# Performance work log

Hardware: AMD Instinct MI355X
Metric: run time of the kernel (lower is better)

## Reference

```python
import jax, jax.numpy as jnp
import numpy as np

NUM_HEADS = 8
EMBED_DIM = 512
HEAD_DIM = EMBED_DIM // NUM_HEADS
SCALE = 1.0 / (HEAD_DIM ** 0.5)


def setup_inputs() -> dict:
    key = jax.random.key(0)
    ks = jax.random.split(key, 8)
    std = 0.02
    x = jax.random.normal(ks[0], (2, 1024, EMBED_DIM), dtype=jnp.float32)
    wq = jax.random.normal(ks[1], (HEAD_DIM, HEAD_DIM), dtype=jnp.float32) * std
    wk = jax.random.normal(ks[2], (HEAD_DIM, HEAD_DIM), dtype=jnp.float32) * std
    wv = jax.random.normal(ks[3], (HEAD_DIM, HEAD_DIM), dtype=jnp.float32) * std
    w1 = jax.random.normal(ks[4], (2 * EMBED_DIM, EMBED_DIM), dtype=jnp.float32) * std
    b1 = jnp.zeros((2 * EMBED_DIM,), dtype=jnp.float32)
    w2 = jax.random.normal(ks[5], (EMBED_DIM, 2 * EMBED_DIM), dtype=jnp.float32) * std
    b2 = jnp.zeros((EMBED_DIM,), dtype=jnp.float32)
    return {"x": x, "wq": wq, "wk": wk, "wv": wv,
            "w1": w1, "b1": b1, "w2": w2, "b2": b2}


def reference(x, wq, wk, wv, w1, b1, w2, b2):
    b, n, e = x.shape
    # rearrange 'b n (h d) -> b (n h) d': heads are folded into the sequence dim,
    # so attention mixes across n*h tokens of head_dim features.
    xh = x.reshape(b, n * NUM_HEADS, HEAD_DIM)  # [b, n*h, d]
    q = jnp.einsum('bsd,ed->bse', xh, wq)
    k = jnp.einsum('bsd,ed->bse', xh, wk)
    v = jnp.einsum('bsd,ed->bse', xh, wv)
    scores = jnp.einsum('bse,bte->bst', q, k) * SCALE  # [b, n*h, n*h]
    attn = jax.nn.softmax(scores, axis=-1)
    out = jnp.einsum('bst,btd->bsd', attn, v)  # [b, n*h, d]
    out = out.reshape(b, n, e)  # 'b (n h) d -> b n (h d)'
    # Mlp: Linear -> GELU(exact) -> Linear (dropout rates are 0)
    h = jax.nn.gelu(jnp.einsum('bne,fe->bnf', out, w1) + b1, approximate=False)
    out = jnp.einsum('bnf,ef->bne', h, w2) + b2
    return attn, out
```

## Files before the change

kernel.cpp:

```cpp
#include <hip/hip_runtime.h>
#include <hip/hip_bf16.h>

typedef __bf16 bf16;
typedef bf16 bf16x8 __attribute__((ext_vector_type(8)));
typedef float f32x16 __attribute__((ext_vector_type(16)));

#define MFMA(a,b,c) __builtin_amdgcn_mfma_f32_32x32x16_bf16(a,b,c,0,0,0)

constexpr int S = 8192;
constexpr long long SB = (long long)S * S;
constexpr long long ATTN_ELEMS = 2 * SB;

__global__ __launch_bounds__(64) void qkv_kernel(
    const float* __restrict__ x, const float* __restrict__ wq,
    const float* __restrict__ wk, const float* __restrict__ wv,
    bf16* __restrict__ qb, bf16* __restrict__ kb, bf16* __restrict__ vt)
{
  __shared__ bf16 vtl[64 * 34];
  const int lane = threadIdx.x;
  const int lo = lane & 31, hi = lane >> 5;
  const int m0 = blockIdx.x * 32;

  bf16x8 af[4];
  {
    const float* xr = x + (size_t)(m0 + lo) * 64 + hi * 8;
#pragma unroll
    for (int s = 0; s < 4; ++s) {
      const float* p = xr + 16 * s;
#pragma unroll
      for (int j = 0; j < 8; ++j) af[s][j] = (bf16)p[j];
    }
  }

  const float* wmats[3] = {wq, wk, wv};
#pragma unroll 1
  for (int mat = 0; mat < 3; ++mat) {
    const float* w = wmats[mat];
#pragma unroll 1
    for (int h = 0; h < 2; ++h) {
      f32x16 acc = {};
#pragma unroll
      for (int s = 0; s < 4; ++s) {
        const float* p = w + (size_t)(32 * h + lo) * 64 + hi * 8 + 16 * s;
        bf16x8 bfr;
#pragma unroll
        for (int j = 0; j < 8; ++j) bfr[j] = (bf16)p[j];
        acc = MFMA(af[s], bfr, acc);
      }
      const int col = 32 * h + lo;
#pragma unroll
      for (int i = 0; i < 16; ++i) {
        int row = (i & 3) + 8 * (i >> 2) + 4 * hi;
        float v = acc[i];
        if (mat == 0) {
          qb[(size_t)(m0 + row) * 64 + col] = (bf16)(v * 0.125f);
        } else if (mat == 1) {
          kb[(size_t)(m0 + row) * 64 + col] = (bf16)v;
        } else {
          vtl[col * 34 + row] = (bf16)v;
        }
      }
    }
  }
  __syncthreads();
  const int b = m0 >> 13;
  const int t0 = m0 & 8191;
#pragma unroll 1
  for (int i = 0; i < 32; ++i) {
    int d = 2 * i + hi;
    vt[(size_t)b * (64 * 8192) + (size_t)d * 8192 + t0 + lo] = vtl[d * 34 + lo];
  }
}

__global__ __launch_bounds__(256) void attn_kernel(
    const bf16* __restrict__ qb, const bf16* __restrict__ kb,
    const bf16* __restrict__ vt, float* __restrict__ attn_out,
    float* __restrict__ o_ws)
{
  __shared__ bf16 plds[4 * 32 * 40];
  __shared__ float olds[32 * 65];
  __shared__ float l4[4 * 32];
  __shared__ float linv[32];

  const int tid = threadIdx.x;
  const int lane = tid & 63;
  const int wt = tid >> 6;
  const int lo = lane & 31, hi = lane >> 5;

  const int bx = blockIdx.x;
  const int g = bx >> 3, r = bx & 7;
  const int b = r >> 2;
  const int m0 = (g * 4 + (r & 3)) * 32;

  for (int i = tid; i < 32 * 65; i += 256) olds[i] = 0.0f;

  bf16x8 qf[4];
  {
    const bf16* qr = qb + ((size_t)b * S + m0 + lo) * 64 + hi * 8;
#pragma unroll
    for (int s = 0; s < 4; ++s) qf[s] = *(const bf16x8*)(qr + 16 * s);
  }
  const bf16* kbase = kb + (size_t)b * S * 64;
  const bf16* vbase = vt + (size_t)b * 64 * S;

  float lsum[16];
#pragma unroll
  for (int i = 0; i < 16; ++i) lsum[i] = 0.0f;
#pragma unroll 1
  for (int c = 0; c < 64; ++c) {
    const int t0 = c * 128 + wt * 32;
    f32x16 acc = {};
#pragma unroll
    for (int s = 0; s < 4; ++s) {
      bf16x8 kf = *(const bf16x8*)(kbase + (size_t)(t0 + lo) * 64 + hi * 8 + 16 * s);
      acc = MFMA(qf[s], kf, acc);
    }
#pragma unroll
    for (int i = 0; i < 16; ++i) lsum[i] += __expf(acc[i]);
  }
#pragma unroll
  for (int i = 0; i < 16; ++i) {
    float v = lsum[i];
#pragma unroll
    for (int m = 1; m <= 16; m <<= 1) v += __shfl_xor(v, m);
    lsum[i] = v;
  }
#pragma unroll
  for (int i = 0; i < 16; ++i)
    if (lo == i) l4[wt * 32 + (i & 3) + 8 * (i >> 2) + 4 * hi] = lsum[i];
  __syncthreads();
  if (tid < 32)
    linv[tid] = 1.0f / (l4[tid] + l4[32 + tid] + l4[64 + tid] + l4[96 + tid]);
  __syncthreads();

  float linv_r[16];
#pragma unroll
  for (int i = 0; i < 16; ++i)
    linv_r[i] = linv[(i & 3) + 8 * (i >> 2) + 4 * hi];

  f32x16 oacc0 = {}, oacc1 = {};
  bf16* pw = plds + wt * 1280;
  float* aout = attn_out + (size_t)b * SB + (size_t)m0 * S;
#pragma unroll 1
  for (int c = 0; c < 64; ++c) {
    const int t0 = c * 128 + wt * 32;
    f32x16 acc = {};
#pragma unroll
    for (int s = 0; s < 4; ++s) {
      bf16x8 kf = *(const bf16x8*)(kbase + (size_t)(t0 + lo) * 64 + hi * 8 + 16 * s);
      acc = MFMA(qf[s], kf, acc);
    }
#pragma unroll
    for (int i = 0; i < 16; ++i) {
      int row = (i & 3) + 8 * (i >> 2) + 4 * hi;
      float p = __expf(acc[i]) * linv_r[i];
      __builtin_nontemporal_store(p, aout + (size_t)row * S + t0 + lo);
      pw[row * 40 + lo] = (bf16)p;
    }
#pragma unroll
    for (int s = 0; s < 2; ++s) {
      bf16x8 pf = *(const bf16x8*)(pw + lo * 40 + 16 * s + 8 * hi);
      bf16x8 v0 = *(const bf16x8*)(vbase + (size_t)lo * S + t0 + 16 * s + 8 * hi);
      bf16x8 v1 = *(const bf16x8*)(vbase + (size_t)(32 + lo) * S + t0 + 16 * s + 8 * hi);
      oacc0 = MFMA(pf, v0, oacc0);
      oacc1 = MFMA(pf, v1, oacc1);
    }
  }
#pragma unroll
  for (int i = 0; i < 16; ++i) {
    int row = (i & 3) + 8 * (i >> 2) + 4 * hi;
    atomicAdd(&olds[row * 65 + lo], oacc0[i]);
    atomicAdd(&olds[row * 65 + 32 + lo], oacc1[i]);
  }
  __syncthreads();
#pragma unroll
  for (int k = 0; k < 8; ++k) {
    int idx = k * 256 + tid;
    int row = idx >> 6, col = idx & 63;
    o_ws[((size_t)b * S + m0 + row) * 64 + col] = olds[row * 65 + col];
  }
}

__device__ inline float gelu_exact(float v) {
  return 0.5f * v * (1.0f + erff(v * 0.70710678118654752f));
}

__global__ __launch_bounds__(256) void mlp1_kernel(
    const float* __restrict__ o_ws, const float* __restrict__ w1,
    const float* __restrict__ b1, bf16* __restrict__ hhi, bf16* __restrict__ hlo)
{
  const int tid = threadIdx.x;
  const int lane = tid & 63;
  const int wid = tid >> 6;
  const int lo = lane & 31, hi = lane >> 5;
  const int mt = blockIdx.x & 31, nt = blockIdx.x >> 5;
  const int m0 = mt * 64 + (wid & 1) * 32;
  const int f0 = nt * 64 + (wid >> 1) * 32;

  f32x16 acc = {};
  const float* arow = o_ws + (size_t)(m0 + lo) * 512 + hi * 8;
  const float* brow = w1 + (size_t)(f0 + lo) * 512 + hi * 8;
#pragma unroll 1
  for (int s = 0; s < 32; ++s) {
    const float* pa = arow + 16 * s;
    const float* pb = brow + 16 * s;
    bf16x8 ah, al, bh, bl;
#pragma unroll
    for (int j = 0; j < 8; ++j) {
      float a = pa[j];  bf16 h = (bf16)a;  ah[j] = h;  al[j] = (bf16)(a - (float)h);
      float bv = pb[j]; bf16 g = (bf16)bv; bh[j] = g;  bl[j] = (bf16)(bv - (float)g);
    }
    acc = MFMA(ah, bh, acc);
    acc = MFMA(ah, bl, acc);
    acc = MFMA(al, bh, acc);
  }
  const int f = f0 + lo;
  const float bias = b1[f];
#pragma unroll
  for (int i = 0; i < 16; ++i) {
    int m = m0 + (i & 3) + 8 * (i >> 2) + 4 * hi;
    float gv = gelu_exact(acc[i] + bias);
    bf16 h = (bf16)gv;
    hhi[(size_t)m * 1024 + f] = h;
    hlo[(size_t)m * 1024 + f] = (bf16)(gv - (float)h);
  }
}

__global__ __launch_bounds__(256) void mlp2_kernel(
    const bf16* __restrict__ hhi, const bf16* __restrict__ hlo,
    const float* __restrict__ w2, const float* __restrict__ b2,
    float* __restrict__ out2)
{
  const int tid = threadIdx.x;
  const int lane = tid & 63;
  const int wid = tid >> 6;
  const int lo = lane & 31, hi = lane >> 5;
  const int mt = blockIdx.x & 31, nt = blockIdx.x >> 5;
  const int m0 = mt * 64 + (wid & 1) * 32;
  const int e0 = nt * 64 + (wid >> 1) * 32;

  f32x16 acc = {};
  const bf16* ahr = hhi + (size_t)(m0 + lo) * 1024 + hi * 8;
  const bf16* alr = hlo + (size_t)(m0 + lo) * 1024 + hi * 8;
  const float* brow = w2 + (size_t)(e0 + lo) * 1024 + hi * 8;
#pragma unroll 1
  for (int s = 0; s < 64; ++s) {
    bf16x8 ah = *(const bf16x8*)(ahr + 16 * s);
    bf16x8 al = *(const bf16x8*)(alr + 16 * s);
    const float* pb = brow + 16 * s;
    bf16x8 bh, bl;
#pragma unroll
    for (int j = 0; j < 8; ++j) {
      float bv = pb[j]; bf16 g = (bf16)bv; bh[j] = g; bl[j] = (bf16)(bv - (float)g);
    }
    acc = MFMA(ah, bh, acc);
    acc = MFMA(al, bh, acc);
    acc = MFMA(ah, bl, acc);
  }
  const int e = e0 + lo;
  const float bias = b2[e];
#pragma unroll
  for (int i = 0; i < 16; ++i) {
    int m = m0 + (i & 3) + 8 * (i >> 2) + 4 * hi;
    out2[(size_t)m * 512 + e] = acc[i] + bias;
  }
}

extern "C" void kernel_launch(void* const* d_in, const int* in_sizes, int n_in,
                              void* d_out, int out_size, void* d_ws, size_t ws_size,
                              hipStream_t stream) {
  const float* x  = (const float*)d_in[0];
  const float* wq = (const float*)d_in[1];
  const float* wk = (const float*)d_in[2];
  const float* wv = (const float*)d_in[3];
  const float* w1 = (const float*)d_in[4];
  const float* b1 = (const float*)d_in[5];
  const float* w2 = (const float*)d_in[6];
  const float* b2 = (const float*)d_in[7];
  float* out = (float*)d_out;

  char* ws = (char*)d_ws;
  bf16* qb   = (bf16*)(ws);
  bf16* kb   = (bf16*)(ws + (2u << 20));
  bf16* vtb  = (bf16*)(ws + (4u << 20));
  float* ob  = (float*)(ws + (6u << 20));
  bf16* hhi  = (bf16*)(ws + (10u << 20));
  bf16* hlo  = (bf16*)(ws + (14u << 20));

  qkv_kernel<<<512, 64, 0, stream>>>(x, wq, wk, wv, qb, kb, vtb);
  attn_kernel<<<512, 256, 0, stream>>>(qb, kb, vtb, out, ob);
  mlp1_kernel<<<512, 256, 0, stream>>>(ob, w1, b1, hhi, hlo);
  mlp2_kernel<<<256, 256, 0, stream>>>(hhi, hlo, w2, b2, out + ATTN_ELEMS);
}
```

Measured before the change: 753.3 us.

## Transpose QK^T MFMA so each lane owns a query row and stores vectorized

Swaps the MFMA operand order so the score tile is computed transposed, making each lane hold 16 key columns of a single query row. This lets the row-sum reduction collapse to a single cross-half shuffle, uses one scalar inverse-sum per lane, and turns the attention-probability writes into 16-byte nontemporal vector stores and 8-byte LDS stores. K and V loads for the tile are also issued up front to hide latency. The main target is the huge fp32 attention-matrix store traffic, which was previously scalar and strided.

```diff
diff --git a/kernel.cpp b/kernel.cpp
--- a/kernel.cpp
+++ b/kernel.cpp
@@ -3,7 +3,9 @@
 
 typedef __bf16 bf16;
 typedef bf16 bf16x8 __attribute__((ext_vector_type(8)));
+typedef bf16 bf16x4 __attribute__((ext_vector_type(4)));
 typedef float f32x16 __attribute__((ext_vector_type(16)));
+typedef float f32x4 __attribute__((ext_vector_type(4)));
 
 #define MFMA(a,b,c) __builtin_amdgcn_mfma_f32_32x32x16_bf16(a,b,c,0,0,0)
 
@@ -103,67 +105,82 @@
   const bf16* kbase = kb + (size_t)b * S * 64;
   const bf16* vbase = vt + (size_t)b * 64 * S;
 
-  float lsum[16];
-#pragma unroll
-  for (int i = 0; i < 16; ++i) lsum[i] = 0.0f;
+  float e0 = 0.0f, e1 = 0.0f, e2 = 0.0f, e3 = 0.0f;
 #pragma unroll 1
   for (int c = 0; c < 64; ++c) {
     const int t0 = c * 128 + wt * 32;
+    const bf16* krow = kbase + (size_t)(t0 + lo) * 64 + hi * 8;
     f32x16 acc = {};
 #pragma unroll
     for (int s = 0; s < 4; ++s) {
-      bf16x8 kf = *(const bf16x8*)(kbase + (size_t)(t0 + lo) * 64 + hi * 8 + 16 * s);
-      acc = MFMA(qf[s], kf, acc);
-    }
-#pragma unroll
-    for (int i = 0; i < 16; ++i) lsum[i] += __expf(acc[i]);
-  }
-#pragma unroll
-  for (int i = 0; i < 16; ++i) {
-    float v = lsum[i];
-#pragma unroll
-    for (int m = 1; m <= 16; m <<= 1) v += __shfl_xor(v, m);
-    lsum[i] = v;
-  }
-#pragma unroll
-  for (int i = 0; i < 16; ++i)
-    if (lo == i) l4[wt * 32 + (i & 3) + 8 * (i >> 2) + 4 * hi] = lsum[i];
+      bf16x8 kf = *(const bf16x8*)(krow + 16 * s);
+      acc = MFMA(kf, qf[s], acc);
+    }
+#pragma unroll
+    for (int i = 0; i < 16; i += 4) {
+      e0 += __expf(acc[i]);
+      e1 += __expf(acc[i + 1]);
+      e2 += __expf(acc[i + 2]);
+      e3 += __expf(acc[i + 3]);
+    }
+  }
+  float lsum = (e0 + e1) + (e2 + e3);
+  lsum += __shfl_xor(lsum, 32);
+  if (hi == 0) l4[wt * 32 + lo] = lsum;
   __syncthreads();
   if (tid < 32)
     linv[tid] = 1.0f / (l4[tid] + l4[32 + tid] + l4[64 + tid] + l4[96 + tid]);
   __syncthreads();
-
-  float linv_r[16];
-#pragma unroll
-  for (int i = 0; i < 16; ++i)
-    linv_r[i] = linv[(i & 3) + 8 * (i >> 2) + 4 * hi];
+  const float li = linv[lo];
 
   f32x16 oacc0 = {}, oacc1 = {};
   bf16* pw = plds + wt * 1280;
   float* aout = attn_out + (size_t)b * SB + (size_t)m0 * S;
+  const size_t rowbase = (size_t)lo * S;
 #pragma unroll 1
   for (int c = 0; c < 64; ++c) {
     const int t0 = c * 128 + wt * 32;
+    const bf16* krow = kbase + (size_t)(t0 + lo) * 64 + hi * 8;
+    bf16x8 kf0 = *(const bf16x8*)(krow);
+    bf16x8 kf1 = *(const bf16x8*)(krow + 16);
+    bf16x8 kf2 = *(const bf16x8*)(krow + 32);
+    bf16x8 kf3 = *(const bf16x8*)(krow + 48);
+    const bf16* vrow = vbase + (size_t)lo * S + t0 + 8 * hi;
+    bf16x8 va0 = *(const bf16x8*)(vrow);
+    bf16x8 va1 = *(const bf16x8*)(vrow + 16);
+    bf16x8 vb0 = *(const bf16x8*)(vrow + (size_t)32 * S);
+    bf16x8 vb1 = *(const bf16x8*)(vrow + (size_t)32 * S + 16);
+
     f32x16 acc = {};
-#pragma unroll
-    for (int s = 0; s < 4; ++s) {
-      bf16x8 kf = *(const bf16x8*)(kbase + (size_t)(t0 + lo) * 64 + hi * 8 + 16 * s);
-      acc = MFMA(qf[s], kf, acc);
-    }
-#pragma unroll
-    for (int i = 0; i < 16; ++i) {
-      int row = (i & 3) + 8 * (i >> 2) + 4 * hi;
-      float p = __expf(acc[i]) * linv_r[i];
-      __builtin_nontemporal_store(p, aout + (size_t)row * S + t0 + lo);
-      pw[row * 40 + lo] = (bf16)p;
+    acc = MFMA(kf0, qf[0], acc);
+    acc = MFMA(kf1, qf[1], acc);
+    acc = MFMA(kf2, qf[2], acc);
+    acc = MFMA(kf3, qf[3], acc);
+
+    float p[16];
+#pragma unroll
+    for (int i = 0; i < 16; ++i) p[i] = __expf(acc[i]) * li;
+
+#pragma unroll
+    for (int gq = 0; gq < 4; ++gq) {
+      bf16x4 pk;
+      pk[0] = (bf16)p[4 * gq];
+      pk[1] = (bf16)p[4 * gq + 1];
+      pk[2] = (bf16)p[4 * gq + 2];
+      pk[3] = (bf16)p[4 * gq + 3];
+      *(bf16x4*)(pw + lo * 40 + 8 * gq + 4 * hi) = pk;
     }
 #pragma unroll
     for (int s = 0; s < 2; ++s) {
       bf16x8 pf = *(const bf16x8*)(pw + lo * 40 + 16 * s + 8 * hi);
-      bf16x8 v0 = *(const bf16x8*)(vbase + (size_t)lo * S + t0 + 16 * s + 8 * hi);
-      bf16x8 v1 = *(const bf16x8*)(vbase + (size_t)(32 + lo) * S + t0 + 16 * s + 8 * hi);
-      oacc0 = MFMA(pf, v0, oacc0);
-      oacc1 = MFMA(pf, v1, oacc1);
+      oacc0 = MFMA(pf, s ? va1 : va0, oacc0);
+      oacc1 = MFMA(pf, s ? vb1 : vb0, oacc1);
+    }
+#pragma unroll
+    for (int gq = 0; gq < 4; ++gq) {
+      f32x4 st = { p[4 * gq], p[4 * gq + 1], p[4 * gq + 2], p[4 * gq + 3] };
+      __builtin_nontemporal_store(st,
+          (f32x4*)(aout + rowbase + t0 + 8 * gq + 4 * hi));
     }
   }
 #pragma unroll
```

New measurement: 1.026 ms. 36.2% more time.

## Prefetch K/V tiles with register double buffering and simplify row-sum reduction

Applied to the files above, without the earlier changes.

The second pass over keys now double-buffers K and V fragments in registers, issuing loads for the next chunk before computing the current one so global-load latency overlaps the MFMA and exp work. The attention-probability stores are moved after the PV MFMAs. The first pass swaps the MFMA operands so each lane's accumulator holds one query row, which replaces the 16-value shuffle reduction with four scalar accumulators and a single cross-half shuffle. The cost is higher register pressure from the extra fragment buffers, which could reduce occupancy.

```diff
diff --git a/kernel.cpp b/kernel.cpp
--- a/kernel.cpp
+++ b/kernel.cpp
@@ -103,31 +103,28 @@
   const bf16* kbase = kb + (size_t)b * S * 64;
   const bf16* vbase = vt + (size_t)b * 64 * S;
 
-  float lsum[16];
-#pragma unroll
-  for (int i = 0; i < 16; ++i) lsum[i] = 0.0f;
+  float e0 = 0.0f, e1 = 0.0f, e2 = 0.0f, e3 = 0.0f;
 #pragma unroll 1
   for (int c = 0; c < 64; ++c) {
     const int t0 = c * 128 + wt * 32;
+    const bf16* krow = kbase + (size_t)(t0 + lo) * 64 + hi * 8;
     f32x16 acc = {};
 #pragma unroll
     for (int s = 0; s < 4; ++s) {
-      bf16x8 kf = *(const bf16x8*)(kbase + (size_t)(t0 + lo) * 64 + hi * 8 + 16 * s);
-      acc = MFMA(qf[s], kf, acc);
-    }
-#pragma unroll
-    for (int i = 0; i < 16; ++i) lsum[i] += __expf(acc[i]);
-  }
-#pragma unroll
-  for (int i = 0; i < 16; ++i) {
-    float v = lsum[i];
-#pragma unroll
-    for (int m = 1; m <= 16; m <<= 1) v += __shfl_xor(v, m);
-    lsum[i] = v;
-  }
-#pragma unroll
-  for (int i = 0; i < 16; ++i)
-    if (lo == i) l4[wt * 32 + (i & 3) + 8 * (i >> 2) + 4 * hi] = lsum[i];
+      bf16x8 kf = *(const bf16x8*)(krow + 16 * s);
+      acc = MFMA(kf, qf[s], acc);
+    }
+#pragma unroll
+    for (int i = 0; i < 16; i += 4) {
+      e0 += __expf(acc[i]);
+      e1 += __expf(acc[i + 1]);
+      e2 += __expf(acc[i + 2]);
+      e3 += __expf(acc[i + 3]);
+    }
+  }
+  float lsum = (e0 + e1) + (e2 + e3);
+  lsum += __shfl_xor(lsum, 32);
+  if (hi == 0) l4[wt * 32 + lo] = lsum;
   __syncthreads();
   if (tid < 32)
     linv[tid] = 1.0f / (l4[tid] + l4[32 + tid] + l4[64 + tid] + l4[96 + tid]);
@@ -141,31 +138,73 @@
   f32x16 oacc0 = {}, oacc1 = {};
   bf16* pw = plds + wt * 1280;
   float* aout = attn_out + (size_t)b * SB + (size_t)m0 * S;
-#pragma unroll 1
-  for (int c = 0; c < 64; ++c) {
-    const int t0 = c * 128 + wt * 32;
+
+  bf16x8 kA[4], vA[4], kB[4], vB[4];
+  {
+    const int t1 = wt * 32;
+    const bf16* krow = kbase + (size_t)(t1 + lo) * 64 + hi * 8;
+    kA[0] = *(const bf16x8*)(krow);
+    kA[1] = *(const bf16x8*)(krow + 16);
+    kA[2] = *(const bf16x8*)(krow + 32);
+    kA[3] = *(const bf16x8*)(krow + 48);
+    const bf16* vrow = vbase + (size_t)lo * S + t1 + 8 * hi;
+    vA[0] = *(const bf16x8*)(vrow);
+    vA[1] = *(const bf16x8*)(vrow + 16);
+    vA[2] = *(const bf16x8*)(vrow + (size_t)32 * S);
+    vA[3] = *(const bf16x8*)(vrow + (size_t)32 * S + 16);
+  }
+
+  auto body = [&](int c_cur, int c_nxt,
+                  bf16x8 (&kc)[4], bf16x8 (&vc)[4],
+                  bf16x8 (&kn)[4], bf16x8 (&vn)[4]) {
+    const int t0 = c_cur * 128 + wt * 32;
+    const int t1 = c_nxt * 128 + wt * 32;
+    const bf16* krow = kbase + (size_t)(t1 + lo) * 64 + hi * 8;
+    kn[0] = *(const bf16x8*)(krow);
+    kn[1] = *(const bf16x8*)(krow + 16);
+    kn[2] = *(const bf16x8*)(krow + 32);
+    kn[3] = *(const bf16x8*)(krow + 48);
+    const bf16* vrow = vbase + (size_t)lo * S + t1 + 8 * hi;
+    vn[0] = *(const bf16x8*)(vrow);
+    vn[1] = *(const bf16x8*)(vrow + 16);
+    vn[2] = *(const bf16x8*)(vrow + (size_t)32 * S);
+    vn[3] = *(const bf16x8*)(vrow + (size_t)32 * S + 16);
+
     f32x16 acc = {};
-#pragma unroll
-    for (int s = 0; s < 4; ++s) {
-      bf16x8 kf = *(const bf16x8*)(kbase + (size_t)(t0 + lo) * 64 + hi * 8 + 16 * s);
-      acc = MFMA(qf[s], kf, acc);
-    }
+    acc = MFMA(qf[0], kc[0], acc);
+    acc = MFMA(qf[1], kc[1], acc);
+    acc = MFMA(qf[2], kc[2], acc);
+    acc = MFMA(qf[3], kc[3], acc);
+
+#pragma unroll
+    for (int i = 0; i < 16; ++i) acc[i] = __expf(acc[i]) * linv_r[i];
+
 #pragma unroll
     for (int i = 0; i < 16; ++i) {
       int row = (i & 3) + 8 * (i >> 2) + 4 * hi;
-      float p = __expf(acc[i]) * linv_r[i];
-      __builtin_nontemporal_store(p, aout + (size_t)row * S + t0 + lo);
-      pw[row * 40 + lo] = (bf16)p;
-    }
-#pragma unroll
-    for (int s = 0; s < 2; ++s) {
-      bf16x8 pf = *(const bf16x8*)(pw + lo * 40 + 16 * s + 8 * hi);
-      bf16x8 v0 = *(const bf16x8*)(vbase + (size_t)lo * S + t0 + 16 * s + 8 * hi);
-      bf16x8 v1 = *(const bf16x8*)(vbase + (size_t)(32 + lo) * S + t0 + 16 * s + 8 * hi);
-      oacc0 = MFMA(pf, v0, oacc0);
-      oacc1 = MFMA(pf, v1, oacc1);
-    }
-  }
+      pw[row * 40 + lo] = (bf16)acc[i];
+    }
+    bf16x8 pf0 = *(const bf16x8*)(pw + lo * 40 + 8 * hi);
+    bf16x8 pf1 = *(const bf16x8*)(pw + lo * 40 + 16 + 8 * hi);
+    oacc0 = MFMA(pf0, vc[0], oacc0);
+    oacc0 = MFMA(pf1, vc[1], oacc0);
+    oacc1 = MFMA(pf0, vc[2], oacc1);
+    oacc1 = MFMA(pf1, vc[3], oacc1);
+
+    float* ab = aout + t0 + lo;
+#pragma unroll
+    for (int i = 0; i < 16; ++i) {
+      int row = (i & 3) + 8 * (i >> 2) + 4 * hi;
+      __builtin_nontemporal_store(acc[i], ab + (size_t)row * S);
+    }
+  };
+
+#pragma unroll 1
+  for (int c = 0; c < 64; c += 2) {
+    body(c, c + 1, kA, vA, kB, vB);
+    body(c + 1, (c + 2) & 63, kB, vB, kA, vA);
+  }
+
 #pragma unroll
   for (int i = 0; i < 16; ++i) {
     int row = (i & 3) + 8 * (i >> 2) + 4 * hi;
```

Result: no change. 749.3 us (-0.5%).
